# Kernel tuning notes

Measured on AMD Instinct MI355X. Metric: run time of the kernel, lower is better.

## Reference

```python
import jax, jax.numpy as jnp
import numpy as np

B, I, D = 512, 128, 64


def setup_inputs() -> dict:
    key = jax.random.key(0)
    embeddings = jax.random.normal(key, (B, I, D), dtype=jnp.float32)
    return {"embeddings": embeddings}


def reference(embeddings):
    # Original: em_ij[b,i,j,d] = emb[b,i,d]*emb[b,j,d]; ctx = mean over j.
    # Algebraically: ctx[b,i,d] = emb[b,i,d] * mean_j emb[b,j,d] -- linear time,
    # no [B,I,I,D] materialization.
    mean_emb = jnp.mean(embeddings, axis=1, keepdims=True)  # [B,1,D]
    ctx_vec = embeddings * mean_emb                         # [B,I,D]
    # activation_function (undefined in the snippet; repo uses a smooth
    # pointwise activation -- tanh assumed). Dropout is identity in eval mode.
    return jnp.tanh(ctx_vec)
```

## Files before the change

### kernel.cpp

```cpp
#include <hip/hip_runtime.h>


#define BB 512
#define II 128
#define DD 64
#define ELEMS_PER_BATCH (II * DD)
#define VEC_PER_BATCH   (ELEMS_PER_BATCH / 4)
#define BLOCK 256
#define VEC_PER_THREAD  (VEC_PER_BATCH / BLOCK)

__device__ __forceinline__ float fast_tanh(float x) {
    float e = __expf(2.0f * x);
    return __fmaf_rn(-2.0f, __builtin_amdgcn_rcpf(e + 1.0f), 1.0f);
}

__global__ __launch_bounds__(BLOCK) void ctx_tanh_kernel(
        const float* __restrict__ emb, float* __restrict__ out) {
    __shared__ float4 s_emb[VEC_PER_BATCH];
    __shared__ float4 s_part[BLOCK];
    __shared__ float4 s_mean[16];

    const int b = blockIdx.x;
    const int t = threadIdx.x;
    const float4* __restrict__ gin  = (const float4*)(emb + (size_t)b * ELEMS_PER_BATCH);
    float4* __restrict__       gout = (float4*)(out + (size_t)b * ELEMS_PER_BATCH);

    float4 acc = make_float4(0.f, 0.f, 0.f, 0.f);
    #pragma unroll
    for (int k = 0; k < VEC_PER_THREAD; ++k) {
        int j = t + BLOCK * k;
        float4 v = gin[j];
        s_emb[j] = v;
        acc.x += v.x; acc.y += v.y; acc.z += v.z; acc.w += v.w;
    }
    s_part[t] = acc;
    __syncthreads();

    if (t < 16) {
        float4 s = make_float4(0.f, 0.f, 0.f, 0.f);
        #pragma unroll
        for (int m = 0; m < 16; ++m) {
            float4 p = s_part[m * 16 + t];
            s.x += p.x; s.y += p.y; s.z += p.z; s.w += p.w;
        }
        const float inv = 1.0f / (float)II;
        s.x *= inv; s.y *= inv; s.z *= inv; s.w *= inv;
        s_mean[t] = s;
    }
    __syncthreads();

    #pragma unroll
    for (int k = 0; k < VEC_PER_THREAD; ++k) {
        int j = t + BLOCK * k;
        float4 v = s_emb[j];
        float4 m = s_mean[j & 15];
        float4 o;
        o.x = fast_tanh(v.x * m.x);
        o.y = fast_tanh(v.y * m.y);
        o.z = fast_tanh(v.z * m.z);
        o.w = fast_tanh(v.w * m.w);
        gout[j] = o;
    }
}

extern "C" void kernel_launch(void* const* d_in, const int* in_sizes, int n_in,
                              void* d_out, int out_size, void* d_ws, size_t ws_size,
                              hipStream_t stream) {
    const float* emb = (const float*)d_in[0];
    float* out = (float*)d_out;
    ctx_tanh_kernel<<<dim3(BB), dim3(BLOCK), 0, stream>>>(emb, out);
}
```

Baseline: 68.27 us.

## Keep batch tile in registers, wave-shuffle reduction, 512-thread blocks, nontemporal stores

Drops the 32KB shared-memory staging of the batch tile and holds each thread's four float4 loads in registers. The column sums are reduced with cross-lane xor shuffles before a small shared-memory combine across waves. Blocks grow to 512 threads with an occupancy hint, and output writes use nontemporal stores to avoid polluting the cache. The aim is to cut LDS traffic and raise occupancy for this memory-bound kernel, at the cost of more registers per thread.

```diff
diff --git a/kernel.cpp b/kernel.cpp
--- a/kernel.cpp
+++ b/kernel.cpp
@@ -6,60 +6,63 @@
 #define DD 64
 #define ELEMS_PER_BATCH (II * DD)
 #define VEC_PER_BATCH   (ELEMS_PER_BATCH / 4)
-#define BLOCK 256
-#define VEC_PER_THREAD  (VEC_PER_BATCH / BLOCK)
+#define BLOCK 512
+#define VPT   (VEC_PER_BATCH / BLOCK)
+#define WAVES (BLOCK / 64)
+
+typedef float f4 __attribute__((ext_vector_type(4)));
 
 __device__ __forceinline__ float fast_tanh(float x) {
     float e = __expf(2.0f * x);
     return __fmaf_rn(-2.0f, __builtin_amdgcn_rcpf(e + 1.0f), 1.0f);
 }
 
-__global__ __launch_bounds__(BLOCK) void ctx_tanh_kernel(
+__global__ __launch_bounds__(BLOCK, 4) void ctx_tanh_kernel(
         const float* __restrict__ emb, float* __restrict__ out) {
-    __shared__ float4 s_emb[VEC_PER_BATCH];
-    __shared__ float4 s_part[BLOCK];
-    __shared__ float4 s_mean[16];
+    __shared__ f4 s_part[WAVES * 16];
+    __shared__ f4 s_mean[16];
 
     const int b = blockIdx.x;
     const int t = threadIdx.x;
-    const float4* __restrict__ gin  = (const float4*)(emb + (size_t)b * ELEMS_PER_BATCH);
-    float4* __restrict__       gout = (float4*)(out + (size_t)b * ELEMS_PER_BATCH);
+    const f4* __restrict__ gin  = (const f4*)(emb + (size_t)b * ELEMS_PER_BATCH);
+    f4* __restrict__       gout = (f4*)(out + (size_t)b * ELEMS_PER_BATCH);
 
-    float4 acc = make_float4(0.f, 0.f, 0.f, 0.f);
+    f4 v[VPT];
     #pragma unroll
-    for (int k = 0; k < VEC_PER_THREAD; ++k) {
-        int j = t + BLOCK * k;
-        float4 v = gin[j];
-        s_emb[j] = v;
-        acc.x += v.x; acc.y += v.y; acc.z += v.z; acc.w += v.w;
-    }
-    s_part[t] = acc;
+    for (int k = 0; k < VPT; ++k) v[k] = gin[t + BLOCK * k];
+
+    f4 acc = v[0];
+    #pragma unroll
+    for (int k = 1; k < VPT; ++k) acc += v[k];
+
+    acc.x += __shfl_xor(acc.x, 16); acc.y += __shfl_xor(acc.y, 16);
+    acc.z += __shfl_xor(acc.z, 16); acc.w += __shfl_xor(acc.w, 16);
+    acc.x += __shfl_xor(acc.x, 32); acc.y += __shfl_xor(acc.y, 32);
+    acc.z += __shfl_xor(acc.z, 32); acc.w += __shfl_xor(acc.w, 32);
+
+    const int lane = t & 63;
+    const int wave = t >> 6;
+    if (lane < 16) s_part[wave * 16 + lane] = acc;
     __syncthreads();
 
     if (t < 16) {
-        float4 s = make_float4(0.f, 0.f, 0.f, 0.f);
+        f4 s = s_part[t];
         #pragma unroll
-        for (int m = 0; m < 16; ++m) {
-            float4 p = s_part[m * 16 + t];
-            s.x += p.x; s.y += p.y; s.z += p.z; s.w += p.w;
-        }
-        const float inv = 1.0f / (float)II;
-        s.x *= inv; s.y *= inv; s.z *= inv; s.w *= inv;
+        for (int w = 1; w < WAVES; ++w) s += s_part[w * 16 + t];
+        s *= (1.0f / (float)II);
         s_mean[t] = s;
     }
     __syncthreads();
 
+    const f4 m4 = s_mean[t & 15];
     #pragma unroll
-    for (int k = 0; k < VEC_PER_THREAD; ++k) {
-        int j = t + BLOCK * k;
-        float4 v = s_emb[j];
-        float4 m = s_mean[j & 15];
-        float4 o;
-        o.x = fast_tanh(v.x * m.x);
-        o.y = fast_tanh(v.y * m.y);
-        o.z = fast_tanh(v.z * m.z);
-        o.w = fast_tanh(v.w * m.w);
-        gout[j] = o;
+    for (int k = 0; k < VPT; ++k) {
+        f4 o;
+        o.x = fast_tanh(v[k].x * m4.x);
+        o.y = fast_tanh(v[k].y * m4.y);
+        o.z = fast_tanh(v[k].z * m4.z);
+        o.w = fast_tanh(v[k].w * m4.w);
+        __builtin_nontemporal_store(o, &gout[t + BLOCK * k]);
     }
 }
 
```

After: 66.14 us. 1.03x faster.
